# Performance work log

Hardware: AMD Instinct MI355X
Metric: run time of the kernel (lower is better)

The kernel has to match this reference:

```python
import jax, jax.numpy as jnp
import numpy as np

B, N_RES, N_ATOMS = 2, 192, 4
N = N_RES * N_ATOMS
NODE_DIM, EDGE_DIM = 128, 64
NUM_AA, NUM_ATOM_TYPES, NUM_PROPS = 20, 4, 30
NUM_RBF, D_MIN, D_MAX = 32, 0.0, 20.0
CUT_OFF = 7.5
AA_EMB, ATOM_EMB, POS_EMB, MUT_OUT = 32, 16, 16, 32
MUT_IN = AA_EMB + AA_EMB + NUM_PROPS + NUM_PROPS          # wt_emb, mut_emb, wt_props, mut_props = 124
NODE_IN = AA_EMB + NUM_PROPS + MUT_OUT + ATOM_EMB + POS_EMB  # 126


def setup_inputs() -> dict:
    key = jax.random.key(0)
    ks = jax.random.split(key, 24)
    s = 0.05
    inp = {
        'coords': jax.random.normal(ks[0], (B, N_RES, N_ATOMS, 3), jnp.float32) * 8.0,
        'mutation_mask': (jax.random.uniform(ks[1], (B, N_RES)) < 0.1).astype(jnp.float32),
        'atom_mask': jnp.ones((B, N_RES, N_ATOMS), jnp.float32),
        'aa_emb': jax.random.normal(ks[2], (NUM_AA, AA_EMB)) * s,
        'atom_emb': jax.random.normal(ks[3], (NUM_ATOM_TYPES, ATOM_EMB)) * s,
        'pos_emb': jax.random.normal(ks[4], (10, POS_EMB)) * s,
        'aa_props': jax.random.normal(ks[5], (NUM_AA, NUM_PROPS)),
        'mut_W1': jax.random.normal(ks[6], (MUT_IN, 64)) * s, 'mut_b1': jnp.zeros((64,)),
        'mut_W2': jax.random.normal(ks[7], (64, MUT_OUT)) * s, 'mut_b2': jnp.zeros((MUT_OUT,)),
        'node_W1': jax.random.normal(ks[8], (NODE_IN, NODE_DIM)) * s, 'node_b1': jnp.zeros((NODE_DIM,)),
        'node_W2': jax.random.normal(ks[9], (NODE_DIM, NODE_DIM)) * s, 'node_b2': jnp.zeros((NODE_DIM,)),
        'edge_W1': jax.random.normal(ks[10], (NUM_RBF, 64)) * s, 'edge_b1': jnp.zeros((64,)),
        'edge_W2': jax.random.normal(ks[11], (64, EDGE_DIM)) * s, 'edge_b2': jnp.zeros((EDGE_DIM,)),
        'wt_indices': jax.random.randint(ks[12], (B, N_RES), 0, NUM_AA),
        'mut_indices': jax.random.randint(ks[13], (B, N_RES), 0, NUM_AA),
        'res_indices': jax.random.randint(ks[14], (B, N), 0, 10),
    }
    return inp


def _mlp2(x, W1, b1, W2, b2):
    return jax.nn.silu(x @ W1 + b1) @ W2 + b2


def reference(coords, mutation_mask, atom_mask, aa_emb, atom_emb, pos_emb, aa_props,
              mut_W1, mut_b1, mut_W2, mut_b2, node_W1, node_b1, node_W2, node_b2,
              edge_W1, edge_b1, edge_W2, edge_b2, wt_indices, mut_indices, res_indices):
    # --- residue-level features ---
    wt_e = aa_emb[wt_indices]        # [B, Nr, 32]
    mut_e = aa_emb[mut_indices]      # [B, Nr, 32]
    wt_p = aa_props[wt_indices]      # [B, Nr, 30]
    mut_p = aa_props[mut_indices]    # [B, Nr, 30]
    mut_in = jnp.concatenate([wt_e, mut_e, wt_p, mut_p], axis=-1)      # [B, Nr, 124]
    mut_feat = _mlp2(mut_in, mut_W1, mut_b1, mut_W2, mut_b2) * mutation_mask[..., None]  # [B, Nr, 32]
    res_feat = jnp.concatenate([wt_e, wt_p, mut_feat], axis=-1)        # [B, Nr, 94]

    # --- per-atom node features ---
    res_tiled = jnp.broadcast_to(res_feat[:, :, None, :], (B, N_RES, N_ATOMS, res_feat.shape[-1]))
    atom_tiled = jnp.broadcast_to(atom_emb[None, None, :, :], (B, N_RES, N_ATOMS, ATOM_EMB))
    flat = jnp.concatenate([res_tiled, atom_tiled], axis=-1).reshape(B, N, -1)
    pos_e = pos_emb[res_indices]                                        # [B, N, 16]
    node_in = jnp.concatenate([flat, pos_e], axis=-1)                   # [B, N, 126]
    atom_mask_flat = atom_mask.reshape(B, N)
    node_features = _mlp2(node_in, node_W1, node_b1, node_W2, node_b2) * atom_mask_flat[..., None]

    # --- dense pairwise edge features ---
    coords_flat = coords.reshape(B, N, 3)
    diff = coords_flat[:, :, None, :] - coords_flat[:, None, :, :]      # [B, N, N, 3]
    dist = jnp.sqrt(jnp.sum(diff * diff, axis=-1) + 1e-8)               # [B, N, N]
    centers = jnp.linspace(D_MIN, D_MAX, NUM_RBF)
    gamma = (D_MAX - D_MIN) / NUM_RBF
    rbf = jnp.exp(-(dist[..., None] - centers) ** 2 / (2.0 * gamma * gamma))  # [B, N, N, 32]
    adj = (dist <= CUT_OFF).astype(jnp.float32)
    adj = adj * atom_mask_flat[:, :, None] * atom_mask_flat[:, None, :]
    adj = adj * (1.0 - jnp.eye(N, dtype=jnp.float32))
    edge_features = _mlp2(rbf, edge_W1, edge_b1, edge_W2, edge_b2) * adj[..., None]  # [B, N, N, 64]

    return node_features, edge_features, coords_flat, atom_mask_flat
```

## Files before the change

### kernel.cpp

```cpp
#include <hip/hip_runtime.h>

#define BB 2
#define NRES 192
#define NATOMS 4
#define NN 768
#define NODE_DIM 128
#define EDGE_DIM 64
#define NUM_RBF 32
#define NROWS (BB * NN)

#define NODE_OFF   ((size_t)0)
#define EDGE_OFF   ((size_t)196608)
#define COORDS_OFF ((size_t)(196608 + 75497472))
#define MASK_OFF   ((size_t)(COORDS_OFF + 4608))

#define WS_NEEDED ((size_t)(NROWS + (size_t)NROWS * NN) * 4)

__device__ __forceinline__ float silu(float x) { return x / (1.0f + expf(-x)); }

__global__ __launch_bounds__(128) void node_kernel(
    const float* __restrict__ coords,
    const float* __restrict__ mut_mask,
    const float* __restrict__ atom_mask,
    const float* __restrict__ aa_emb,
    const float* __restrict__ atom_emb,
    const float* __restrict__ pos_emb,
    const float* __restrict__ aa_props,
    const float* __restrict__ mW1, const float* __restrict__ mb1,
    const float* __restrict__ mW2, const float* __restrict__ mb2,
    const float* __restrict__ nW1, const float* __restrict__ nb1,
    const float* __restrict__ nW2, const float* __restrict__ nb2,
    const int* __restrict__ wt_idx, const int* __restrict__ mut_idx,
    const int* __restrict__ res_idx,
    float* __restrict__ out)
{
    __shared__ float s_in[128];
    __shared__ float s_h[128];
    __shared__ float s_res[96];
    __shared__ float s_nin[128];

    const int blk = blockIdx.x;
    const int t = threadIdx.x;

    const int wt = wt_idx[blk];
    const int mu = mut_idx[blk];
    const float mm = mut_mask[blk];

    if (t < 32) { s_in[t] = aa_emb[wt * 32 + t]; s_in[32 + t] = aa_emb[mu * 32 + t]; }
    if (t < 30) { s_in[64 + t] = aa_props[wt * 30 + t]; s_in[94 + t] = aa_props[mu * 30 + t]; }
    __syncthreads();

    if (t < 64) {
        float acc = mb1[t];
        for (int k = 0; k < 124; ++k) acc += s_in[k] * mW1[k * 64 + t];
        s_h[t] = silu(acc);
    }
    __syncthreads();

    if (t < 32) {
        float acc = mb2[t];
        for (int k = 0; k < 64; ++k) acc += s_h[k] * mW2[k * 32 + t];
        s_res[62 + t] = acc * mm;
        s_res[t] = s_in[t];
    }
    if (t < 30) s_res[32 + t] = s_in[64 + t];
    __syncthreads();

    for (int a = 0; a < 4; ++a) {
        const int gn = blk * 4 + a;
        if (t < 94) s_nin[t] = s_res[t];
        else if (t < 110) s_nin[t] = atom_emb[a * 16 + (t - 94)];
        else if (t < 126) s_nin[t] = pos_emb[res_idx[gn] * 16 + (t - 110)];
        __syncthreads();

        float acc = nb1[t];
        for (int k = 0; k < 126; ++k) acc += s_nin[k] * nW1[k * 128 + t];
        float h = silu(acc);
        __syncthreads();
        s_h[t] = h;
        __syncthreads();

        float o = nb2[t];
        for (int k = 0; k < 128; ++k) o += s_h[k] * nW2[k * 128 + t];
        const float am = atom_mask[gn];
        out[NODE_OFF + (size_t)gn * 128 + t] = o * am;
        __syncthreads();
    }

    if (t < 12) out[COORDS_OFF + (size_t)blk * 12 + t] = coords[(size_t)blk * 12 + t];
    if (t < 4)  out[MASK_OFF + (size_t)blk * 4 + t]  = atom_mask[(size_t)blk * 4 + t];
}

__global__ __launch_bounds__(256) void pair_kernel(
    const float* __restrict__ coords,
    const float* __restrict__ atom_mask,
    int* __restrict__ ws)
{
    __shared__ int s_list[NN];
    __shared__ int s_cnt;

    const int row = blockIdx.x;
    const int b = row / NN;
    const int i = row % NN;
    const int t = threadIdx.x;
    const int lane = t & 63;

    if (t == 0) s_cnt = 0;
    __syncthreads();

    const float* cb = coords + (size_t)b * NN * 3;
    const float* mb = atom_mask + (size_t)b * NN;
    const float xi = cb[i * 3 + 0], yi = cb[i * 3 + 1], zi = cb[i * 3 + 2];
    const float mi = mb[i];

    for (int r = 0; r < 3; ++r) {
        const int j = t + r * 256;
        const float dx = xi - cb[j * 3 + 0];
        const float dy = yi - cb[j * 3 + 1];
        const float dz = zi - cb[j * 3 + 2];
        const float d2 = dx * dx + dy * dy + dz * dz + 1e-8f;
        const float mprod = mi * mb[j];
        const bool adj = (d2 <= 7.5f * 7.5f) && (j != i) && (mprod != 0.0f);
        const unsigned long long bal = __ballot(adj);
        const int lofs = __popcll(bal & ((1ull << lane) - 1ull));
        int base = 0;
        if (lane == 0 && bal) base = atomicAdd(&s_cnt, __popcll(bal));
        base = __shfl(base, 0);
        if (adj) s_list[base + lofs] = j;
    }
    __syncthreads();

    const int cnt = s_cnt;
    if (t == 0) ws[row] = cnt;
    int* listp = ws + NROWS + (size_t)row * NN;
    for (int q = t; q < cnt; q += 256) listp[q] = s_list[q];
}

__global__ __launch_bounds__(256) void mlp_kernel(
    const float* __restrict__ coords,
    const float* __restrict__ atom_mask,
    const float* __restrict__ eW1, const float* __restrict__ eb1,
    const float* __restrict__ eW2, const float* __restrict__ eb2,
    const int* __restrict__ ws,
    float* __restrict__ out)
{
    const int row = blockIdx.x;
    const int cnt = ws[row];
    if (cnt == 0) return;

    const int b = row / NN;
    const int i = row % NN;
    const int t = threadIdx.x;

    const float* cb = coords + (size_t)b * NN * 3;
    const float* mb = atom_mask + (size_t)b * NN;
    const float xi = cb[i * 3 + 0], yi = cb[i * 3 + 1], zi = cb[i * 3 + 2];
    const float mi = mb[i];
    const int* listp = ws + NROWS + (size_t)row * NN;
    float* rowp = out + EDGE_OFF + (size_t)row * (size_t)NN * EDGE_DIM;

    for (int idx = t; idx < cnt; idx += 256) {
        const int j = listp[idx];
        const float dx = xi - cb[j * 3 + 0];
        const float dy = yi - cb[j * 3 + 1];
        const float dz = zi - cb[j * 3 + 2];
        const float d = sqrtf(dx * dx + dy * dy + dz * dz + 1e-8f);
        const float mf = mi * mb[j];

        float rbf[NUM_RBF];
        #pragma unroll
        for (int k = 0; k < NUM_RBF; ++k) {
            const float dd = d - (float)k * (20.0f / 31.0f);
            rbf[k] = expf(-(dd * dd) / 0.78125f);
        }

        float o[EDGE_DIM];
        #pragma unroll
        for (int c = 0; c < EDGE_DIM; c += 4) {
            const float4 bb4 = *(const float4*)&eb2[c];
            o[c] = bb4.x; o[c + 1] = bb4.y; o[c + 2] = bb4.z; o[c + 3] = bb4.w;
        }

        for (int h = 0; h < 64; ++h) {
            float acc = eb1[h];
            #pragma unroll
            for (int k = 0; k < NUM_RBF; ++k) acc += rbf[k] * eW1[k * 64 + h];
            const float hv = silu(acc);
            #pragma unroll
            for (int c = 0; c < EDGE_DIM; c += 4) {
                const float4 w4 = *(const float4*)&eW2[h * 64 + c];
                o[c]     += hv * w4.x;
                o[c + 1] += hv * w4.y;
                o[c + 2] += hv * w4.z;
                o[c + 3] += hv * w4.w;
            }
        }

        float* pp = rowp + (size_t)j * EDGE_DIM;
        #pragma unroll
        for (int q = 0; q < EDGE_DIM / 4; ++q) {
            ((float4*)pp)[q] = make_float4(o[4 * q] * mf, o[4 * q + 1] * mf,
                                           o[4 * q + 2] * mf, o[4 * q + 3] * mf);
        }
    }
}

__global__ __launch_bounds__(256) void edge_fused_kernel(
    const float* __restrict__ coords,
    const float* __restrict__ atom_mask,
    const float* __restrict__ eW1, const float* __restrict__ eb1,
    const float* __restrict__ eW2, const float* __restrict__ eb2,
    float* __restrict__ out)
{
    __shared__ float xs[NN], ys[NN], zs[NN], ms[NN];
    __shared__ float W1[NUM_RBF * 64];
    __shared__ float W2[64 * 64];
    __shared__ float b1[64], b2[64];

    const int blk = blockIdx.x;
    const int b = blk / NN;
    const int i = blk % NN;
    const int t = threadIdx.x;

    const float* cb = coords + (size_t)b * NN * 3;
    for (int n = t; n < NN; n += 256) {
        xs[n] = cb[n * 3 + 0];
        ys[n] = cb[n * 3 + 1];
        zs[n] = cb[n * 3 + 2];
        ms[n] = atom_mask[(size_t)b * NN + n];
    }
    for (int k = t; k < NUM_RBF * 64; k += 256) W1[k] = eW1[k];
    for (int k = t; k < 64 * 64; k += 256)      W2[k] = eW2[k];
    if (t < 64) { b1[t] = eb1[t]; b2[t] = eb2[t]; }
    __syncthreads();

    const int lane = t & 63;
    const int wv = t >> 6;
    const float xi = xs[i], yi = ys[i], zi = zs[i], mi = ms[i];
    float* rowp = out + EDGE_OFF + ((size_t)b * NN + i) * (size_t)NN * EDGE_DIM;

    for (int g = wv; g < NN / 8; g += 4) {
        const int j0 = g * 8;
        const int jj = j0 + (lane & 7);
        const float dx = xi - xs[jj];
        const float dy = yi - ys[jj];
        const float dz = zi - zs[jj];
        const float dist = sqrtf(dx * dx + dy * dy + dz * dz + 1e-8f);
        const float mprod = mi * ms[jj];
        const bool adj = (dist <= 7.5f) && (jj != i) && (mprod != 0.0f);
        const unsigned long long bal = __ballot(adj && (lane < 8));
        float* gp = rowp + (size_t)j0 * EDGE_DIM;

        if (bal == 0ULL) {
            ((uint4*)gp)[lane] = make_uint4(0u, 0u, 0u, 0u);
            ((uint4*)gp)[lane + 64] = make_uint4(0u, 0u, 0u, 0u);
        } else {
            for (int p = 0; p < 8; ++p) {
                float* pp = gp + p * EDGE_DIM;
                if ((bal >> p) & 1ULL) {
                    const float d = __shfl(dist, p);
                    const float mf = __shfl(mprod, p);
                    const float ck = (float)(lane & 31) * (20.0f / 31.0f);
                    const float dd = d - ck;
                    const float my_r = expf(-(dd * dd) / 0.78125f);
                    float acc = b1[lane];
                    #pragma unroll
                    for (int k = 0; k < 32; ++k) {
                        const float rk = __shfl(my_r, k);
                        acc += rk * W1[k * 64 + lane];
                    }
                    const float h = silu(acc);
                    float o = b2[lane];
                    for (int hh = 0; hh < 64; ++hh) {
                        const float hv = __shfl(h, hh);
                        o += hv * W2[hh * 64 + lane];
                    }
                    pp[lane] = o * mf;
                } else {
                    ((unsigned int*)pp)[lane] = 0u;
                }
            }
        }
    }
}

extern "C" void kernel_launch(void* const* d_in, const int* in_sizes, int n_in,
                              void* d_out, int out_size, void* d_ws, size_t ws_size,
                              hipStream_t stream) {
    const float* coords    = (const float*)d_in[0];
    const float* mut_mask  = (const float*)d_in[1];
    const float* atom_mask = (const float*)d_in[2];
    const float* aa_emb    = (const float*)d_in[3];
    const float* atom_emb  = (const float*)d_in[4];
    const float* pos_emb   = (const float*)d_in[5];
    const float* aa_props  = (const float*)d_in[6];
    const float* mut_W1    = (const float*)d_in[7];
    const float* mut_b1    = (const float*)d_in[8];
    const float* mut_W2    = (const float*)d_in[9];
    const float* mut_b2    = (const float*)d_in[10];
    const float* node_W1   = (const float*)d_in[11];
    const float* node_b1   = (const float*)d_in[12];
    const float* node_W2   = (const float*)d_in[13];
    const float* node_b2   = (const float*)d_in[14];
    const float* edge_W1   = (const float*)d_in[15];
    const float* edge_b1   = (const float*)d_in[16];
    const float* edge_W2   = (const float*)d_in[17];
    const float* edge_b2   = (const float*)d_in[18];
    const int* wt_indices  = (const int*)d_in[19];
    const int* mut_indices = (const int*)d_in[20];
    const int* res_indices = (const int*)d_in[21];

    float* out = (float*)d_out;

    if (ws_size >= WS_NEEDED) {
        hipMemsetAsync(d_out, 0, (size_t)out_size * sizeof(float), stream);
        node_kernel<<<BB * NRES, 128, 0, stream>>>(
            coords, mut_mask, atom_mask, aa_emb, atom_emb, pos_emb, aa_props,
            mut_W1, mut_b1, mut_W2, mut_b2, node_W1, node_b1, node_W2, node_b2,
            wt_indices, mut_indices, res_indices, out);
        pair_kernel<<<NROWS, 256, 0, stream>>>(coords, atom_mask, (int*)d_ws);
        mlp_kernel<<<NROWS, 256, 0, stream>>>(
            coords, atom_mask, edge_W1, edge_b1, edge_W2, edge_b2,
            (const int*)d_ws, out);
    } else {
        node_kernel<<<BB * NRES, 128, 0, stream>>>(
            coords, mut_mask, atom_mask, aa_emb, atom_emb, pos_emb, aa_props,
            mut_W1, mut_b1, mut_W2, mut_b2, node_W1, node_b1, node_W2, node_b2,
            wt_indices, mut_indices, res_indices, out);
        edge_fused_kernel<<<NROWS, 256, 0, stream>>>(
            coords, atom_mask, edge_W1, edge_b1, edge_W2, edge_b2, out);
    }
}
```

Baseline: 140.3 us.

## Compact sparse edge MLP into workspace and scatter with single streaming write

Replaces the full-output memset plus pair/mlp kernels with a sparse kernel that builds a per-row slot map and computes edge MLPs for adjacent pairs into a compacted workspace. A separate write kernel then fills the whole edge output once, using nontemporal stores of zeros or the gathered values. This removes the double write of the large edge tensor (memset, then scatter). The cost is a large workspace and an extra read of the slot map. It also splits the first-layer dot product into four accumulators for ILP and drops the fused fallback kernel, so the code needs workspace to produce edge output.

```diff
diff --git a/kernel.cpp b/kernel.cpp
--- a/kernel.cpp
+++ b/kernel.cpp
@@ -14,7 +14,11 @@
 #define COORDS_OFF ((size_t)(196608 + 75497472))
 #define MASK_OFF   ((size_t)(COORDS_OFF + 4608))
 
-#define WS_NEEDED ((size_t)(NROWS + (size_t)NROWS * NN) * 4)
+#define SLOTMAP_INTS ((size_t)NROWS * NN)
+#define WS_MAIN_NEEDED ((SLOTMAP_INTS * 4) + ((size_t)NROWS * NN * EDGE_DIM * 4))
+#define WS_FALLBACK_NEEDED ((size_t)(NROWS + (size_t)NROWS * NN) * 4)
+
+typedef unsigned int u32x4 __attribute__((ext_vector_type(4)));
 
 __device__ __forceinline__ float silu(float x) { return x / (1.0f + expf(-x)); }
 
@@ -91,6 +95,128 @@
     if (t < 4)  out[MASK_OFF + (size_t)blk * 4 + t]  = atom_mask[(size_t)blk * 4 + t];
 }
 
+__global__ __launch_bounds__(256) void sparse_kernel(
+    const float* __restrict__ coords,
+    const float* __restrict__ atom_mask,
+    const float* __restrict__ eW1, const float* __restrict__ eb1,
+    const float* __restrict__ eW2, const float* __restrict__ eb2,
+    int* __restrict__ slotmap,
+    float* __restrict__ wsdata)
+{
+    __shared__ int s_list[NN];
+    __shared__ int s_cnt;
+
+    const int row = blockIdx.x;
+    const int b = row / NN;
+    const int i = row % NN;
+    const int t = threadIdx.x;
+    const int lane = t & 63;
+
+    if (t == 0) s_cnt = 0;
+    __syncthreads();
+
+    const float* cb = coords + (size_t)b * NN * 3;
+    const float* mb = atom_mask + (size_t)b * NN;
+    const float xi = cb[i * 3 + 0], yi = cb[i * 3 + 1], zi = cb[i * 3 + 2];
+    const float mi = mb[i];
+    int* smrow = slotmap + (size_t)row * NN;
+
+    for (int r = 0; r < 3; ++r) {
+        const int j = t + r * 256;
+        const float dx = xi - cb[j * 3 + 0];
+        const float dy = yi - cb[j * 3 + 1];
+        const float dz = zi - cb[j * 3 + 2];
+        const float d2 = dx * dx + dy * dy + dz * dz + 1e-8f;
+        const float mprod = mi * mb[j];
+        const bool adj = (d2 <= 7.5f * 7.5f) && (j != i) && (mprod != 0.0f);
+        const unsigned long long bal = __ballot(adj);
+        const int lofs = __popcll(bal & ((1ull << lane) - 1ull));
+        int base = 0;
+        if (lane == 0 && bal) base = atomicAdd(&s_cnt, __popcll(bal));
+        base = __shfl(base, 0);
+        const int slot = base + lofs;
+        smrow[j] = adj ? slot : -1;
+        if (adj) s_list[slot] = j;
+    }
+    __syncthreads();
+
+    const int cnt = s_cnt;
+    float* drow = wsdata + (size_t)row * NN * EDGE_DIM;
+
+    for (int idx = t; idx < cnt; idx += 256) {
+        const int j = s_list[idx];
+        const float dx = xi - cb[j * 3 + 0];
+        const float dy = yi - cb[j * 3 + 1];
+        const float dz = zi - cb[j * 3 + 2];
+        const float d = sqrtf(dx * dx + dy * dy + dz * dz + 1e-8f);
+        const float mf = mi * mb[j];
+
+        float rbf[NUM_RBF];
+        #pragma unroll
+        for (int k = 0; k < NUM_RBF; ++k) {
+            const float dd = d - (float)k * (20.0f / 31.0f);
+            rbf[k] = expf(-(dd * dd) / 0.78125f);
+        }
+
+        float o[EDGE_DIM];
+        #pragma unroll
+        for (int c = 0; c < EDGE_DIM; c += 4) {
+            const float4 bb4 = *(const float4*)&eb2[c];
+            o[c] = bb4.x; o[c + 1] = bb4.y; o[c + 2] = bb4.z; o[c + 3] = bb4.w;
+        }
+
+        for (int h = 0; h < 64; ++h) {
+            float a0 = 0.f, a1 = 0.f, a2 = 0.f, a3 = 0.f;
+            #pragma unroll
+            for (int k = 0; k < NUM_RBF; k += 4) {
+                a0 += rbf[k]     * eW1[(k)     * 64 + h];
+                a1 += rbf[k + 1] * eW1[(k + 1) * 64 + h];
+                a2 += rbf[k + 2] * eW1[(k + 2) * 64 + h];
+                a3 += rbf[k + 3] * eW1[(k + 3) * 64 + h];
+            }
+            const float hv = silu(eb1[h] + ((a0 + a1) + (a2 + a3)));
+            #pragma unroll
+            for (int c = 0; c < EDGE_DIM; c += 4) {
+                const float4 w4 = *(const float4*)&eW2[h * 64 + c];
+                o[c]     += hv * w4.x;
+                o[c + 1] += hv * w4.y;
+                o[c + 2] += hv * w4.z;
+                o[c + 3] += hv * w4.w;
+            }
+        }
+
+        float* pp = drow + (size_t)idx * EDGE_DIM;
+        #pragma unroll
+        for (int q = 0; q < EDGE_DIM / 4; ++q) {
+            ((float4*)pp)[q] = make_float4(o[4 * q] * mf, o[4 * q + 1] * mf,
+                                           o[4 * q + 2] * mf, o[4 * q + 3] * mf);
+        }
+    }
+}
+
+__global__ __launch_bounds__(256) void write_kernel(
+    const int* __restrict__ slotmap,
+    const float* __restrict__ wsdata,
+    float* __restrict__ out)
+{
+    const size_t total = (size_t)NROWS * NN * (EDGE_DIM / 4);
+    u32x4* ep = (u32x4*)(out + EDGE_OFF);
+    const u32x4 z4 = {0u, 0u, 0u, 0u};
+
+    for (size_t q = (size_t)blockIdx.x * 256 + threadIdx.x; q < total;
+         q += (size_t)gridDim.x * 256) {
+        const size_t subrow = q >> 4;
+        const int slot = slotmap[subrow];
+        u32x4 v = z4;
+        if (slot >= 0) {
+            const size_t row = subrow / NN;
+            const u32x4* sp = (const u32x4*)(wsdata + (row * NN + (size_t)slot) * EDGE_DIM);
+            v = sp[q & 15];
+        }
+        __builtin_nontemporal_store(v, &ep[q]);
+    }
+}
+
 __global__ __launch_bounds__(256) void pair_kernel(
     const float* __restrict__ coords,
     const float* __restrict__ atom_mask,
@@ -182,10 +308,15 @@
         }
 
         for (int h = 0; h < 64; ++h) {
-            float acc = eb1[h];
+            float a0 = 0.f, a1 = 0.f, a2 = 0.f, a3 = 0.f;
             #pragma unroll
-            for (int k = 0; k < NUM_RBF; ++k) acc += rbf[k] * eW1[k * 64 + h];
-            const float hv = silu(acc);
+            for (int k = 0; k < NUM_RBF; k += 4) {
+                a0 += rbf[k]     * eW1[(k)     * 64 + h];
+                a1 += rbf[k + 1] * eW1[(k + 1) * 64 + h];
+                a2 += rbf[k + 2] * eW1[(k + 2) * 64 + h];
+                a3 += rbf[k + 3] * eW1[(k + 3) * 64 + h];
+            }
+            const float hv = silu(eb1[h] + ((a0 + a1) + (a2 + a3)));
             #pragma unroll
             for (int c = 0; c < EDGE_DIM; c += 4) {
                 const float4 w4 = *(const float4*)&eW2[h * 64 + c];
@@ -201,85 +332,6 @@
         for (int q = 0; q < EDGE_DIM / 4; ++q) {
             ((float4*)pp)[q] = make_float4(o[4 * q] * mf, o[4 * q + 1] * mf,
                                            o[4 * q + 2] * mf, o[4 * q + 3] * mf);
-        }
-    }
-}
-
-__global__ __launch_bounds__(256) void edge_fused_kernel(
-    const float* __restrict__ coords,
-    const float* __restrict__ atom_mask,
-    const float* __restrict__ eW1, const float* __restrict__ eb1,
-    const float* __restrict__ eW2, const float* __restrict__ eb2,
-    float* __restrict__ out)
-{
-    __shared__ float xs[NN], ys[NN], zs[NN], ms[NN];
-    __shared__ float W1[NUM_RBF * 64];
-    __shared__ float W2[64 * 64];
-    __shared__ float b1[64], b2[64];
-
-    const int blk = blockIdx.x;
-    const int b = blk / NN;
-    const int i = blk % NN;
-    const int t = threadIdx.x;
-
-    const float* cb = coords + (size_t)b * NN * 3;
-    for (int n = t; n < NN; n += 256) {
-        xs[n] = cb[n * 3 + 0];
-        ys[n] = cb[n * 3 + 1];
-        zs[n] = cb[n * 3 + 2];
-        ms[n] = atom_mask[(size_t)b * NN + n];
-    }
-    for (int k = t; k < NUM_RBF * 64; k += 256) W1[k] = eW1[k];
-    for (int k = t; k < 64 * 64; k += 256)      W2[k] = eW2[k];
-    if (t < 64) { b1[t] = eb1[t]; b2[t] = eb2[t]; }
-    __syncthreads();
-
-    const int lane = t & 63;
-    const int wv = t >> 6;
-    const float xi = xs[i], yi = ys[i], zi = zs[i], mi = ms[i];
-    float* rowp = out + EDGE_OFF + ((size_t)b * NN + i) * (size_t)NN * EDGE_DIM;
-
-    for (int g = wv; g < NN / 8; g += 4) {
-        const int j0 = g * 8;
-        const int jj = j0 + (lane & 7);
-        const float dx = xi - xs[jj];
-        const float dy = yi - ys[jj];
-        const float dz = zi - zs[jj];
-        const float dist = sqrtf(dx * dx + dy * dy + dz * dz + 1e-8f);
-        const float mprod = mi * ms[jj];
-        const bool adj = (dist <= 7.5f) && (jj != i) && (mprod != 0.0f);
-        const unsigned long long bal = __ballot(adj && (lane < 8));
-        float* gp = rowp + (size_t)j0 * EDGE_DIM;
-
-        if (bal == 0ULL) {
-            ((uint4*)gp)[lane] = make_uint4(0u, 0u, 0u, 0u);
-            ((uint4*)gp)[lane + 64] = make_uint4(0u, 0u, 0u, 0u);
-        } else {
-            for (int p = 0; p < 8; ++p) {
-                float* pp = gp + p * EDGE_DIM;
-                if ((bal >> p) & 1ULL) {
-                    const float d = __shfl(dist, p);
-                    const float mf = __shfl(mprod, p);
-                    const float ck = (float)(lane & 31) * (20.0f / 31.0f);
-                    const float dd = d - ck;
-                    const float my_r = expf(-(dd * dd) / 0.78125f);
-                    float acc = b1[lane];
-                    #pragma unroll
-                    for (int k = 0; k < 32; ++k) {
-                        const float rk = __shfl(my_r, k);
-                        acc += rk * W1[k * 64 + lane];
-                    }
-                    const float h = silu(acc);
-                    float o = b2[lane];
-                    for (int hh = 0; hh < 64; ++hh) {
-                        const float hv = __shfl(h, hh);
-                        o += hv * W2[hh * 64 + lane];
-                    }
-                    pp[lane] = o * mf;
-                } else {
-                    ((unsigned int*)pp)[lane] = 0u;
-                }
-            }
         }
     }
 }
@@ -312,22 +364,24 @@
 
     float* out = (float*)d_out;
 
-    if (ws_size >= WS_NEEDED) {
-        hipMemsetAsync(d_out, 0, (size_t)out_size * sizeof(float), stream);
-        node_kernel<<<BB * NRES, 128, 0, stream>>>(
-            coords, mut_mask, atom_mask, aa_emb, atom_emb, pos_emb, aa_props,
-            mut_W1, mut_b1, mut_W2, mut_b2, node_W1, node_b1, node_W2, node_b2,
-            wt_indices, mut_indices, res_indices, out);
+    node_kernel<<<BB * NRES, 128, 0, stream>>>(
+        coords, mut_mask, atom_mask, aa_emb, atom_emb, pos_emb, aa_props,
+        mut_W1, mut_b1, mut_W2, mut_b2, node_W1, node_b1, node_W2, node_b2,
+        wt_indices, mut_indices, res_indices, out);
+
+    if (ws_size >= WS_MAIN_NEEDED) {
+        int* slotmap = (int*)d_ws;
+        float* wsdata = (float*)((char*)d_ws + SLOTMAP_INTS * 4);
+        sparse_kernel<<<NROWS, 256, 0, stream>>>(
+            coords, atom_mask, edge_W1, edge_b1, edge_W2, edge_b2,
+            slotmap, wsdata);
+        write_kernel<<<2048, 256, 0, stream>>>(slotmap, wsdata, out);
+    } else if (ws_size >= WS_FALLBACK_NEEDED) {
+        (void)hipMemsetAsync((char*)d_out + EDGE_OFF * 4,
+                             0, (size_t)NROWS * NN * EDGE_DIM * 4, stream);
         pair_kernel<<<NROWS, 256, 0, stream>>>(coords, atom_mask, (int*)d_ws);
         mlp_kernel<<<NROWS, 256, 0, stream>>>(
             coords, atom_mask, edge_W1, edge_b1, edge_W2, edge_b2,
             (const int*)d_ws, out);
-    } else {
-        node_kernel<<<BB * NRES, 128, 0, stream>>>(
-            coords, mut_mask, atom_mask, aa_emb, atom_emb, pos_emb, aa_props,
-            mut_W1, mut_b1, mut_W2, mut_b2, node_W1, node_b1, node_W2, node_b2,
-            wt_indices, mut_indices, res_indices, out);
-        edge_fused_kernel<<<NROWS, 256, 0, stream>>>(
-            coords, atom_mask, edge_W1, edge_b1, edge_W2, edge_b2, out);
-    }
-}
+    }
+}
```

After: 150.8 us. +7.5%, slower.
